# Kernel tuning notes

Hardware: AMD Instinct MI355X
Metric: run time of the kernel (lower is better)

The kernel has to match this reference:

```python
import jax, jax.numpy as jnp
import numpy as np

LN_EPS = 1e-12


def layer_norm(x, g, b):
    mu = jnp.mean(x, axis=-1, keepdims=True)
    var = jnp.mean(jnp.square(x - mu), axis=-1, keepdims=True)
    return (x - mu) * jax.lax.rsqrt(var + LN_EPS) * g + b


def setup_inputs() -> dict:
    key = jax.random.key(0)
    ks = jax.random.split(key, 12)
    B, L, H, P, V = 8, 512, 768, 200, 30522
    src_scores = jax.random.normal(ks[0], (B, L, L), jnp.float32)
    seq_hidden = jax.random.normal(ks[1], (B, L, H), jnp.float32)
    seq_mask = jax.random.randint(ks[2], (B, L), 0, 2).astype(jnp.float32)
    pos_emb = jax.random.normal(ks[3], (512, P), jnp.float32) * 0.02
    Wp = jax.random.normal(ks[4], (H, P), jnp.float32) * 0.02
    bp = jnp.zeros((H,), jnp.float32)
    Wt = jax.random.normal(ks[5], (H, H), jnp.float32) * 0.02
    bt = jnp.zeros((H,), jnp.float32)
    ln_g = jnp.ones((H,), jnp.float32)
    ln_b = jnp.zeros((H,), jnp.float32)
    Wd = jax.random.normal(ks[6], (V, H), jnp.float32) * 0.02
    dec_bias = jnp.zeros((V,), jnp.float32)
    return dict(src_scores=src_scores, seq_hidden=seq_hidden, seq_mask=seq_mask,
                pos_emb=pos_emb, Wp=Wp, bp=bp, Wt=Wt, bt=bt,
                ln_g=ln_g, ln_b=ln_b, Wd=Wd, dec_bias=dec_bias)


def reference(src_scores, seq_hidden, seq_mask, pos_emb, Wp, bp, Wt, bt, ln_g, ln_b, Wd, dec_bias):
    L = src_scores.shape[1]
    # position embeddings for first L positions, projected to hidden size: [L, H]
    pos_h = pos_emb[:L] @ Wp.T + bp
    # pos_scores[b, l, s] = pos_h[l] . seq_hidden[b, s]
    pos_scores = jnp.einsum('lh,bsh->bls', pos_h, seq_hidden)
    scores = pos_scores + src_scores + seq_mask[:, None, :] * -10000.0
    alpha = jax.nn.softmax(scores, axis=-1)                 # [B, L, L]
    seq_sum = jnp.einsum('bls,bsh->blh', alpha, seq_hidden)  # [B, L, H]
    # BertPredictionHeadTransform: dense -> gelu (exact) -> LayerNorm
    h = layer_norm(jax.nn.gelu(seq_sum @ Wt.T + bt, approximate=False), ln_g, ln_b)
    target_scores = h @ Wd.T + dec_bias                      # [B, L, V]
    return target_scores
```

## Files before the change

### kernel.cpp

```cpp
#include <hip/hip_runtime.h>

using f32x4  = __attribute__((ext_vector_type(4))) float;
using short8 = __attribute__((ext_vector_type(8))) short;
using short4v= __attribute__((ext_vector_type(4))) short;
typedef __attribute__((ext_vector_type(8))) __bf16 bf16x8;

__device__ static inline short f2bf(float f){
    unsigned u = __builtin_bit_cast(unsigned, f);
    u += 0x7fffu + ((u >> 16) & 1u);
    return (short)(u >> 16);
}

__device__ static inline void gload_lds16(const void* g, void* l){
    __builtin_amdgcn_global_load_lds(
        (const __attribute__((address_space(1))) void*)g,
        (__attribute__((address_space(3))) void*)l, 16, 0, 0);
}

#define BKK 64

template<int EPI, bool T2D>
__global__ __launch_bounds__(256, 2)
void gemm_bt(const short* __restrict__ A, const short* __restrict__ B,
             float* __restrict__ outF, short* __restrict__ outB,
             const float* __restrict__ bias,
             const float* __restrict__ addmat, const float* __restrict__ mask,
             int K, int ldc, int Ncheck,
             long sA, long sB, long sC, long sX, int maskStride)
{
    __shared__ short Abuf[128*BKK];
    __shared__ short Bbuf[128*BKK];
    const int tid  = threadIdx.x;
    const int wave = tid >> 6;
    const int lane = tid & 63;
    const int bz   = blockIdx.z;

    int bx = blockIdx.x, by = blockIdx.y;
    if constexpr (T2D) {
        const int GX = gridDim.x, GY = gridDim.y;
        const int f  = blockIdx.y * GX + blockIdx.x;
        const int nfull  = GX >> 3;
        const int fullsz = (nfull << 3) * GY;
        int mg, mloc, nloc, nbase;
        if (f < fullsz) {
            const int band = f / (GY << 3);
            const int r    = f - band * (GY << 3);
            mg   = r >> 6;
            const int rr = r & 63;
            mloc = rr & 7; nloc = rr >> 3;
            nbase = band << 3;
        } else {
            const int rem = GX & 7;
            const int fp  = f - fullsz;
            const int gsz = rem << 3;
            mg   = fp / gsz;
            const int rr = fp - mg * gsz;
            mloc = rr & 7; nloc = rr >> 3;
            nbase = nfull << 3;
        }
        bx = nbase + nloc;
        by = (mg << 3) + mloc;
    }
    const int m0 = by * 128;
    const int n0 = bx * 128;
    const short* Ab = A + (long)bz * sA;
    const short* Bb = B + (long)bz * sB;

    const int wr = (wave >> 1) * 64;
    const int wc = (wave &  1) * 64;

    f32x4 acc[4][4];
    #pragma unroll
    for (int i=0;i<4;++i)
        #pragma unroll
        for (int j=0;j<4;++j) acc[i][j] = (f32x4){0.f,0.f,0.f,0.f};

    const int srow = wave*32 + (lane >> 3);
    const int kch  = (lane & 7) ^ (lane >> 3);
    const short* gA = Ab + (long)(m0 + srow)*K + kch*8;
    const short* gB = Bb + (long)(n0 + srow)*K + kch*8;
    short* lA = Abuf + wave*32*BKK;
    short* lB = Bbuf + wave*32*BKK;

    for (int k0 = 0; k0 < K; k0 += BKK) {
        __syncthreads();
        #pragma unroll
        for (int is=0; is<4; ++is){
            gload_lds16(gA + k0 + (long)is*8*K, lA + is*8*BKK);
            gload_lds16(gB + k0 + (long)is*8*K, lB + is*8*BKK);
        }
        __syncthreads();
        #pragma unroll
        for (int ks=0; ks<2; ++ks){
            bf16x8 af[4], bfr[4];
            const int chunk = ks*4 + (lane >> 4);
            #pragma unroll
            for (int mi=0;mi<4;++mi){
                int row = wr + mi*16 + (lane & 15);
                af[mi] = *(const bf16x8*)((const char*)Abuf + row*128 + ((chunk ^ (row & 7))<<4));
            }
            #pragma unroll
            for (int ni=0;ni<4;++ni){
                int row = wc + ni*16 + (lane & 15);
                bfr[ni] = *(const bf16x8*)((const char*)Bbuf + row*128 + ((chunk ^ (row & 7))<<4));
            }
            #pragma unroll
            for (int mi=0;mi<4;++mi)
                #pragma unroll
                for (int ni=0;ni<4;++ni)
                    acc[mi][ni] = __builtin_amdgcn_mfma_f32_16x16x32_bf16(af[mi], bfr[ni], acc[mi][ni], 0, 0, 0);
        }
    }

    const int rb = (lane >> 4) * 4;
    const int cb = lane & 15;
    #pragma unroll
    for (int mi=0;mi<4;++mi){
        #pragma unroll
        for (int r=0;r<4;++r){
            const int row = m0 + wr + mi*16 + rb + r;
            #pragma unroll
            for (int ni=0;ni<4;++ni){
                const int col = n0 + wc + ni*16 + cb;
                float v = acc[mi][ni][r];
                if constexpr (EPI == 0) {
                    v += addmat[(long)bz*sX + (long)row*ldc + col]
                         - 10000.f * mask[bz*maskStride + col];
                    outF[(long)bz*sC + (long)row*ldc + col] = v;
                } else if constexpr (EPI == 1) {
                    outB[(long)bz*sC + (long)row*ldc + col] = f2bf(v);
                } else if constexpr (EPI == 3) {
                    if (col < Ncheck) outF[(long)row*ldc + col] = v + bias[col];
                } else if constexpr (EPI == 4) {
                    outB[(long)row*ldc + col] = f2bf(v + bias[col]);
                }
            }
        }
    }
}

template<bool T2D>
__global__ __launch_bounds__(512, 2)
void gemm_bt256(const short* __restrict__ A, const short* __restrict__ B,
                float* __restrict__ outF, const float* __restrict__ bias,
                int K, int ldc, int Ncheck, int maxBrow)
{
    __shared__ __align__(16) short Abuf[2][256*32];
    __shared__ __align__(16) short Bbuf[2][256*32];
    const int tid  = threadIdx.x;
    const int wave = tid >> 6;
    const int lane = tid & 63;

    int bx = blockIdx.x, by = blockIdx.y;
    if constexpr (T2D) {
        const int GX = gridDim.x, GY = gridDim.y;
        const int f  = blockIdx.y * GX + blockIdx.x;
        const int band = f / (GY << 3);
        const int r2   = f - band * (GY << 3);
        const int mg   = r2 >> 6;
        const int rr   = r2 & 63;
        bx = (band << 3) + (rr >> 3);
        by = (mg << 3) + (rr & 7);
    }
    const int m0 = by * 256;
    const int n0 = bx * 256;

    const int wr = (wave >> 2) * 128;
    const int wc = (wave & 3) * 64;

    f32x4 acc[8][4];
    #pragma unroll
    for (int i=0;i<8;++i)
        #pragma unroll
        for (int j=0;j<4;++j) acc[i][j] = (f32x4){0.f,0.f,0.f,0.f};

    const int srow = wave*16 + (lane >> 2);
    const int kch  = (lane & 3) ^ ((lane >> 3) & 3);
    const short* gA0 = A + (long)(m0 + srow)       * K + kch*8;
    const short* gA1 = A + (long)(m0 + 128 + srow) * K + kch*8;
    int br0 = n0 + srow;        if (br0 > maxBrow) br0 = maxBrow;
    int br1 = n0 + 128 + srow;  if (br1 > maxBrow) br1 = maxBrow;
    const short* gB0 = B + (long)br0 * K + kch*8;
    const short* gB1 = B + (long)br1 * K + kch*8;
    const int lofs = wave*16*32;

    const int nt = K / 32;

    auto STAGE = [&](int buf, int t){
        const long k0 = (long)t * 32;
        gload_lds16(gA0 + k0, &Abuf[buf][lofs]);
        gload_lds16(gA1 + k0, &Abuf[buf][128*32 + lofs]);
        gload_lds16(gB0 + k0, &Bbuf[buf][lofs]);
        gload_lds16(gB1 + k0, &Bbuf[buf][128*32 + lofs]);
    };

    STAGE(0, 0);

    const int qsl = (((lane >> 4) ^ ((lane >> 1) & 3)) << 4);
    const int rA  = wr + (lane & 15);
    const int rB  = wc + (lane & 15);

    for (int t = 0; t < nt; ++t) {
        const int cur = t & 1, nxt = cur ^ 1;
        __builtin_amdgcn_s_barrier();
        if (t + 1 < nt) {
            STAGE(nxt, t + 1);
            asm volatile("s_waitcnt vmcnt(4)" ::: "memory");
        } else {
            asm volatile("s_waitcnt vmcnt(0)" ::: "memory");
        }
        __builtin_amdgcn_s_barrier();
        asm volatile("" ::: "memory");

        bf16x8 af[8], bfr[4];
        #pragma unroll
        for (int ni=0;ni<4;++ni)
            bfr[ni] = *(const bf16x8*)((const char*)&Bbuf[cur][0] + (rB + ni*16)*64 + qsl);
        #pragma unroll
        for (int mi=0;mi<8;++mi)
            af[mi]  = *(const bf16x8*)((const char*)&Abuf[cur][0] + (rA + mi*16)*64 + qsl);
        #pragma unroll
        for (int mi=0;mi<8;++mi)
            #pragma unroll
            for (int ni=0;ni<4;++ni)
                acc[mi][ni] = __builtin_amdgcn_mfma_f32_16x16x32_bf16(af[mi], bfr[ni], acc[mi][ni], 0, 0, 0);
    }

    const int rb = (lane >> 4) * 4;
    const int cb = lane & 15;
    #pragma unroll
    for (int mi=0;mi<8;++mi){
        #pragma unroll
        for (int r=0;r<4;++r){
            const long row = (long)m0 + wr + mi*16 + rb + r;
            #pragma unroll
            for (int ni=0;ni<4;++ni){
                const int col = n0 + wc + ni*16 + cb;
                if (col < Ncheck)
                    outF[row*ldc + col] = acc[mi][ni][r] + bias[col];
            }
        }
    }
}

__global__ __launch_bounds__(256)
void conv_bf16(const float* __restrict__ in, short* __restrict__ out, long n, long ntot)
{
    const long stride = (long)gridDim.x * 2048;
    for (long i = ((long)blockIdx.x*256 + threadIdx.x)*8; i < ntot; i += stride){
        short8 o = (short8){0,0,0,0,0,0,0,0};
        if (i < n){
            f32x4 a = *(const f32x4*)(in + i);
            f32x4 b = *(const f32x4*)(in + i + 4);
            o[0]=f2bf(a[0]); o[1]=f2bf(a[1]); o[2]=f2bf(a[2]); o[3]=f2bf(a[3]);
            o[4]=f2bf(b[0]); o[5]=f2bf(b[1]); o[6]=f2bf(b[2]); o[7]=f2bf(b[3]);
        }
        *(short8*)(out + i) = o;
    }
}

__global__ __launch_bounds__(256)
void conv_pad(const float* __restrict__ in, short* __restrict__ out,
              int Cin, int Cpad, int total)
{
    int idx = blockIdx.x*256 + threadIdx.x;
    if (idx >= total) return;
    int r = idx / Cpad, c = idx - r*Cpad;
    short v = 0;
    if (c < Cin) v = f2bf(in[(long)r*Cin + c]);
    out[idx] = v;
}

__global__ __launch_bounds__(256)
void transpose_to_bf16(const float* __restrict__ in, short* __restrict__ out, int R, int C)
{
    __shared__ float t[32][33];
    const long boff = (long)blockIdx.z * R * C;
    const float* inb = in + boff;
    short* outb = out + boff;
    int c0 = blockIdx.x*32, r0 = blockIdx.y*32;
    int tx = threadIdx.x & 31, ty = threadIdx.x >> 5;
    #pragma unroll
    for (int j=0;j<32;j+=8) t[ty+j][tx] = inb[(long)(r0+ty+j)*C + c0+tx];
    __syncthreads();
    #pragma unroll
    for (int j=0;j<32;j+=8) outb[(long)(c0+ty+j)*R + r0+tx] = f2bf(t[tx][ty+j]);
}

__global__ __launch_bounds__(256)
void softmax_bf16(const float* __restrict__ scores, short* __restrict__ alpha, int L)
{
    const int row  = blockIdx.x*4 + (threadIdx.x >> 6);
    const int lane = threadIdx.x & 63;
    const float* p = scores + (long)row*L + lane*8;
    f32x4 v0 = *(const f32x4*)p;
    f32x4 v1 = *(const f32x4*)(p+4);
    float x[8] = {v0[0],v0[1],v0[2],v0[3],v1[0],v1[1],v1[2],v1[3]};
    float m = x[0];
    #pragma unroll
    for (int j=1;j<8;++j) m = fmaxf(m, x[j]);
    #pragma unroll
    for (int off=32; off; off>>=1) m = fmaxf(m, __shfl_xor(m, off));
    float s = 0.f;
    #pragma unroll
    for (int j=0;j<8;++j){ x[j] = __expf(x[j]-m); s += x[j]; }
    #pragma unroll
    for (int off=32; off; off>>=1) s += __shfl_xor(s, off);
    const float rinv = 1.f / s;
    short8 o;
    #pragma unroll
    for (int j=0;j<8;++j) o[j] = f2bf(x[j]*rinv);
    *(short8*)(alpha + (long)row*L + lane*8) = o;
}

__global__ __launch_bounds__(256)
void gelu_ln(const float* __restrict__ lin, short* __restrict__ h,
             const float* __restrict__ g, const float* __restrict__ b, int H)
{
    const int row  = blockIdx.x*4 + (threadIdx.x >> 6);
    const int lane = threadIdx.x & 63;
    const float* p = lin + (long)row*H;
    float x[12];
    #pragma unroll
    for (int c=0;c<3;++c){
        f32x4 v = *(const f32x4*)(p + c*256 + lane*4);
        x[c*4+0]=v[0]; x[c*4+1]=v[1]; x[c*4+2]=v[2]; x[c*4+3]=v[3];
    }
    float sum=0.f, sq=0.f;
    #pragma unroll
    for (int j=0;j<12;++j){
        float t = 0.5f * x[j] * (1.f + erff(x[j]*0.70710678118654752f));
        x[j] = t; sum += t; sq += t*t;
    }
    #pragma unroll
    for (int off=32; off; off>>=1){ sum += __shfl_xor(sum, off); sq += __shfl_xor(sq, off); }
    const float mu  = sum * (1.f/768.f);
    const float var = sq  * (1.f/768.f) - mu*mu;
    const float inv = rsqrtf(var + 1e-12f);
    #pragma unroll
    for (int c=0;c<3;++c){
        short4v o;
        #pragma unroll
        for (int j=0;j<4;++j){
            int col = c*256 + lane*4 + j;
            o[j] = f2bf((x[c*4+j]-mu)*inv*g[col] + b[col]);
        }
        *(short4v*)(h + (long)row*H + c*256 + lane*4) = o;
    }
}

extern "C" void kernel_launch(void* const* d_in, const int* in_sizes, int n_in,
                              void* d_out, int out_size, void* d_ws, size_t ws_size,
                              hipStream_t stream)
{
    const float* src_scores = (const float*)d_in[0];
    const float* seq_hidden = (const float*)d_in[1];
    const float* seq_mask   = (const float*)d_in[2];
    const float* pos_emb    = (const float*)d_in[3];
    const float* Wp         = (const float*)d_in[4];
    const float* bp         = (const float*)d_in[5];
    const float* Wt         = (const float*)d_in[6];
    const float* bt         = (const float*)d_in[7];
    const float* ln_g       = (const float*)d_in[8];
    const float* ln_b       = (const float*)d_in[9];
    const float* Wd         = (const float*)d_in[10];
    const float* dec_bias   = (const float*)d_in[11];
    float* out = (float*)d_out;

    const int B=8, L=512, H=768, V=30522, Vp=30592, Kp=256;

    const size_t need = ((size_t)Vp*H + (size_t)B*L*H) * sizeof(short);
    if (ws_size < need) return;
    short* wd_bf = (short*)d_ws;
    short* h_bf  = wd_bf + (long)Vp*H;

    char* sc = (char*)d_out;
    short* sh_nat = (short*)sc;  sc += (long)B*L*H*2;
    short* sh_t   = (short*)sc;  sc += (long)B*L*H*2;
    short* pe_p   = (short*)sc;  sc += (long)L*Kp*2;
    short* wp_p   = (short*)sc;  sc += (long)H*Kp*2;
    short* pos_h  = (short*)sc;  sc += (long)L*H*2;
    short* wt_bf  = (short*)sc;  sc += (long)H*H*2;
    float* scoresb= (float*)sc;  sc += (long)B*L*L*4;
    short* alpha  = (short*)sc;  sc += (long)B*L*L*2;
    short* seqsum = (short*)sc;  sc += (long)B*L*H*2;
    float* lin5   = (float*)sc;  sc += (long)B*L*H*4;

    {   long n=(long)V*H, ntot=(long)Vp*H;
        int blocks=(int)((ntot+2047)/2048); if (blocks>2048) blocks=2048;
        conv_bf16<<<dim3(blocks),256,0,stream>>>(Wd, wd_bf, n, ntot); }
    {   long n=(long)H*H; int blocks=(int)((n+2047)/2048);
        conv_bf16<<<dim3(blocks),256,0,stream>>>(Wt, wt_bf, n, n); }
    {   long n=(long)B*L*H; int blocks=(int)((n+2047)/2048); if (blocks>2048) blocks=2048;
        conv_bf16<<<dim3(blocks),256,0,stream>>>(seq_hidden, sh_nat, n, n); }
    transpose_to_bf16<<<dim3(H/32, L/32, B),256,0,stream>>>(seq_hidden, sh_t, L, H);
    {   int total=L*Kp;
        conv_pad<<<dim3((total+255)/256),256,0,stream>>>(pos_emb, pe_p, 200, Kp, total); }
    {   int total=H*Kp;
        conv_pad<<<dim3((total+255)/256),256,0,stream>>>(Wp, wp_p, 200, Kp, total); }

    gemm_bt<4,false><<<dim3(H/128, L/128, 1),256,0,stream>>>(
        pe_p, wp_p, nullptr, pos_h, bp, nullptr, nullptr,
        Kp, H, H, 0L, 0L, 0L, 0L, 0);

    gemm_bt<0,false><<<dim3(L/128, L/128, B),256,0,stream>>>(
        pos_h, sh_nat, scoresb, nullptr, nullptr, src_scores, seq_mask,
        H, L, L, 0L, (long)L*H, (long)L*L, (long)L*L, L);

    softmax_bf16<<<dim3(B*L/4),256,0,stream>>>(scoresb, alpha, L);

    gemm_bt<1,false><<<dim3(H/128, L/128, B),256,0,stream>>>(
        alpha, sh_t, nullptr, seqsum, nullptr, nullptr, nullptr,
        L, H, H, (long)L*L, (long)H*L, (long)L*H, 0L, 0);

    gemm_bt<3,false><<<dim3(H/128, (B*L)/128, 1),256,0,stream>>>(
        seqsum, wt_bf, lin5, nullptr, bt, nullptr, nullptr,
        H, H, H, 0L, 0L, 0L, 0L, 0);

    gelu_ln<<<dim3(B*L/4),256,0,stream>>>(lin5, h_bf, ln_g, ln_b, H);

    gemm_bt256<true><<<dim3(120, 16), 512, 0, stream>>>(
        h_bf, wd_bf, out, dec_bias, H, V, V, Vp - 1);
}
```

Measured before the change: 557.5 us.

## Restructure decoder GEMM into ping-pong pipelined K-64 stages with setprio

Rewrites the large vocabulary-projection GEMM to process K in 64-wide steps split into two 32-wide halves, double-buffered. Loads for the next step are issued piecewise between MFMA phases, separated by explicit barriers, with s_setprio raised around the MFMA blocks. Occupancy drops to one block per CU because LDS use doubles. The goal is to hide global-to-LDS latency and LDS read latency behind matrix math, at the cost of more barriers and lower occupancy.

```diff
diff --git a/kernel.cpp b/kernel.cpp
--- a/kernel.cpp
+++ b/kernel.cpp
@@ -16,6 +16,8 @@
         (const __attribute__((address_space(1))) void*)g,
         (__attribute__((address_space(3))) void*)l, 16, 0, 0);
 }
+
+#define BARM() asm volatile("s_barrier" ::: "memory")
 
 #define BKK 64
 
@@ -140,13 +142,13 @@
 }
 
 template<bool T2D>
-__global__ __launch_bounds__(512, 2)
-void gemm_bt256(const short* __restrict__ A, const short* __restrict__ B,
-                float* __restrict__ outF, const float* __restrict__ bias,
-                int K, int ldc, int Ncheck, int maxBrow)
-{
-    __shared__ __align__(16) short Abuf[2][256*32];
-    __shared__ __align__(16) short Bbuf[2][256*32];
+__global__ __launch_bounds__(512, 1)
+void gemm_bt256p(const short* __restrict__ A, const short* __restrict__ B,
+                 float* __restrict__ outF, const float* __restrict__ bias,
+                 int K, int ldc, int Ncheck, int maxBrow)
+{
+    __shared__ __align__(16) short Ab[2][2][256*32];
+    __shared__ __align__(16) short Bb[2][2][256*32];
     const int tid  = threadIdx.x;
     const int wave = tid >> 6;
     const int lane = tid & 63;
@@ -175,55 +177,72 @@
         for (int j=0;j<4;++j) acc[i][j] = (f32x4){0.f,0.f,0.f,0.f};
 
     const int srow = wave*16 + (lane >> 2);
-    const int kch  = (lane & 3) ^ ((lane >> 3) & 3);
-    const short* gA0 = A + (long)(m0 + srow)       * K + kch*8;
-    const short* gA1 = A + (long)(m0 + 128 + srow) * K + kch*8;
+    const int cg   = (lane & 3) ^ ((lane >> 3) & 3);
+    const short* gA0 = A + (long)(m0 + srow)       * K + cg*8;
+    const short* gA1 = gA0 + (long)128 * K;
     int br0 = n0 + srow;        if (br0 > maxBrow) br0 = maxBrow;
     int br1 = n0 + 128 + srow;  if (br1 > maxBrow) br1 = maxBrow;
-    const short* gB0 = B + (long)br0 * K + kch*8;
-    const short* gB1 = B + (long)br1 * K + kch*8;
-    const int lofs = wave*16*32;
-
-    const int nt = K / 32;
-
-    auto STAGE = [&](int buf, int t){
-        const long k0 = (long)t * 32;
-        gload_lds16(gA0 + k0, &Abuf[buf][lofs]);
-        gload_lds16(gA1 + k0, &Abuf[buf][128*32 + lofs]);
-        gload_lds16(gB0 + k0, &Bbuf[buf][lofs]);
-        gload_lds16(gB1 + k0, &Bbuf[buf][128*32 + lofs]);
-    };
-
-    STAGE(0, 0);
-
-    const int qsl = (((lane >> 4) ^ ((lane >> 1) & 3)) << 4);
-    const int rA  = wr + (lane & 15);
-    const int rB  = wc + (lane & 15);
+    const short* gB0 = B + (long)br0 * K + cg*8;
+    const short* gB1 = B + (long)br1 * K + cg*8;
+    const int so = wave*16*32;
+
+    const int nt = K / 64;
+
+    #define SA(bb,kh,kc) { gload_lds16(gA0 + (kc) + (kh)*32, &Ab[bb][kh][so]); \
+                           gload_lds16(gA1 + (kc) + (kh)*32, &Ab[bb][kh][128*32 + so]); }
+    #define SB(bb,kh,kc) { gload_lds16(gB0 + (kc) + (kh)*32, &Bb[bb][kh][so]); \
+                           gload_lds16(gB1 + (kc) + (kh)*32, &Bb[bb][kh][128*32 + so]); }
+
+    const int ch   = (lane >> 4) ^ ((lane >> 1) & 3);
+    const int aoff = (wr + (lane & 15))*32 + ch*8;
+    const int boff = (wc + (lane & 15))*32 + ch*8;
+
+    SA(0,0,0); SB(0,0,0); SA(0,1,0); SB(0,1,0);
+    asm volatile("s_waitcnt vmcnt(4)" ::: "memory");
+    BARM();
 
     for (int t = 0; t < nt; ++t) {
-        const int cur = t & 1, nxt = cur ^ 1;
-        __builtin_amdgcn_s_barrier();
-        if (t + 1 < nt) {
-            STAGE(nxt, t + 1);
-            asm volatile("s_waitcnt vmcnt(4)" ::: "memory");
-        } else {
-            asm volatile("s_waitcnt vmcnt(0)" ::: "memory");
-        }
-        __builtin_amdgcn_s_barrier();
-        asm volatile("" ::: "memory");
-
-        bf16x8 af[8], bfr[4];
-        #pragma unroll
-        for (int ni=0;ni<4;++ni)
-            bfr[ni] = *(const bf16x8*)((const char*)&Bbuf[cur][0] + (rB + ni*16)*64 + qsl);
-        #pragma unroll
-        for (int mi=0;mi<8;++mi)
-            af[mi]  = *(const bf16x8*)((const char*)&Abuf[cur][0] + (rA + mi*16)*64 + qsl);
-        #pragma unroll
-        for (int mi=0;mi<8;++mi)
-            #pragma unroll
-            for (int ni=0;ni<4;++ni)
-                acc[mi][ni] = __builtin_amdgcn_mfma_f32_16x16x32_bf16(af[mi], bfr[ni], acc[mi][ni], 0, 0, 0);
+        const int buf = t & 1, nb = buf ^ 1;
+        const bool pf = (t + 1) < nt;
+        const long kc = (long)(t + 1) * 64;
+        bf16x8 af[8], bq[2];
+
+        #define RDA(kh) { _Pragma("unroll") \
+            for (int mi=0;mi<8;++mi) af[mi] = *(const bf16x8*)&Ab[buf][kh][aoff + mi*512]; }
+        #define RDB(kh,n0i) { bq[0] = *(const bf16x8*)&Bb[buf][kh][boff + (n0i)*512]; \
+                              bq[1] = *(const bf16x8*)&Bb[buf][kh][boff + (n0i+1)*512]; }
+        #define MF(n0i) { __builtin_amdgcn_s_setprio(1); _Pragma("unroll") \
+            for (int mi=0;mi<8;++mi){ \
+                acc[mi][n0i]   = __builtin_amdgcn_mfma_f32_16x16x32_bf16(af[mi], bq[0], acc[mi][n0i],   0,0,0); \
+                acc[mi][n0i+1] = __builtin_amdgcn_mfma_f32_16x16x32_bf16(af[mi], bq[1], acc[mi][n0i+1], 0,0,0); } \
+            __builtin_amdgcn_s_setprio(0); }
+
+        RDA(0); RDB(0,0);
+        if (pf) SA(nb,0,kc);
+        BARM();
+        MF(0);
+        BARM();
+        RDB(0,2);
+        if (pf) { SB(nb,0,kc); asm volatile("s_waitcnt vmcnt(4)" ::: "memory"); }
+        else    {              asm volatile("s_waitcnt vmcnt(0)" ::: "memory"); }
+        BARM();
+        MF(2);
+        BARM();
+        RDA(1); RDB(1,0);
+        if (pf) SA(nb,1,kc);
+        BARM();
+        MF(0);
+        BARM();
+        RDB(1,2);
+        if (pf) { SB(nb,1,kc); asm volatile("s_waitcnt vmcnt(4)" ::: "memory"); }
+        else    {              asm volatile("s_waitcnt vmcnt(0)" ::: "memory"); }
+        BARM();
+        MF(2);
+        BARM();
+
+        #undef RDA
+        #undef RDB
+        #undef MF
     }
 
     const int rb = (lane >> 4) * 4;
@@ -419,6 +438,6 @@
 
     gelu_ln<<<dim3(B*L/4),256,0,stream>>>(lin5, h_bf, ln_g, ln_b, H);
 
-    gemm_bt256<true><<<dim3(120, 16), 512, 0, stream>>>(
+    gemm_bt256p<true><<<dim3(120, 16), 512, 0, stream>>>(
         h_bf, wd_bf, out, dec_bias, H, V, V, Vp - 1);
 }
```

Measured after the change: 481.8 us. 13.6% less time.
